# Kernel tuning notes

Hardware: AMD Instinct MI355X
Metric: run time of the kernel (lower is better)

## Reference

```python
import jax, jax.numpy as jnp
import numpy as np

N = 40000; E = 500000; IN = 128; ED = 16; HID = 64; HEADS = 4; OUT = 256; B = 128
NEG = 0.2  # GATv2 leaky_relu negative slope


def _add_self_loops(edge_index, edge_attr, n):
    # PyG add_self_loops with fill_value='mean': loop attr = mean of incoming edge attrs per node
    dst = edge_index[1]
    s = jax.ops.segment_sum(edge_attr, dst, num_segments=n)
    c = jax.ops.segment_sum(jnp.ones((edge_attr.shape[0],), edge_attr.dtype), dst, num_segments=n)
    loop_attr = s / jnp.maximum(c, 1.0)[:, None]
    loops = jnp.arange(n, dtype=edge_index.dtype)
    ei = jnp.concatenate([edge_index, jnp.stack([loops, loops])], axis=1)
    ea = jnp.concatenate([edge_attr, loop_attr], axis=0)
    return ei, ea


def _seg_softmax(logits, seg, n):
    m = jax.ops.segment_max(logits, seg, num_segments=n)
    m = jnp.where(jnp.isfinite(m), m, 0.0)  # guard empty segments
    e = jnp.exp(logits - m[seg])
    z = jax.ops.segment_sum(e, seg, num_segments=n)
    return e / (z[seg] + 1e-16)


def _gatv2(x, src, dst, ea, Wl, bl, Wr, br, We, att, bias, heads, oc, concat):
    n = x.shape[0]
    xl = (x @ Wl + bl).reshape(n, heads, oc)  # lin_l (source/message transform)
    xr = (x @ Wr + br).reshape(n, heads, oc)  # lin_r (target transform)
    ef = (ea @ We).reshape(-1, heads, oc)     # lin_edge (no bias)
    s = jax.nn.leaky_relu(xl[src] + xr[dst] + ef, NEG)  # [Etot,H,C]
    alpha = _seg_softmax(jnp.einsum('ehc,hc->eh', s, att), dst, n)  # scatter-softmax over dst
    out = jax.ops.segment_sum(xl[src] * alpha[..., None], dst, num_segments=n)  # [N,H,C]
    out = out.reshape(n, heads * oc) if concat else out.mean(axis=1)
    return out + bias


def setup_inputs():
    ks = jax.random.split(jax.random.key(0), 32)
    W = lambda i, shp: jax.random.normal(ks[i], shp, jnp.float32) * 0.05
    z = lambda d: jnp.zeros((d,), jnp.float32)
    H = HEADS * HID
    return dict(
        x=jax.random.normal(ks[0], (N, IN), jnp.float32),
        edge_index=jax.random.randint(ks[1], (2, E), 0, N),
        edge_attr=jax.random.normal(ks[2], (E, ED), jnp.float32),
        batch=jnp.sort(jax.random.randint(ks[3], (N,), 0, B)),
        batch_size=B,
        c1_Wl=W(4, (IN, H)), c1_bl=z(H), c1_Wr=W(5, (IN, H)), c1_br=z(H), c1_We=W(6, (ED, H)), c1_att=W(7, (HEADS, HID)), c1_bias=z(H),
        c2_Wl=W(8, (H, H)), c2_bl=z(H), c2_Wr=W(9, (H, H)), c2_br=z(H), c2_We=W(10, (ED, H)), c2_att=W(11, (HEADS, HID)), c2_bias=z(H),
        c3_Wl=W(12, (H, OUT)), c3_bl=z(OUT), c3_Wr=W(13, (H, OUT)), c3_br=z(OUT), c3_We=W(14, (ED, OUT)), c3_att=W(15, (1, OUT)), c3_bias=z(OUT),
        gate_W1=W(16, (OUT, 128)), gate_b1=z(128), gate_W2=W(17, (128, 1)), gate_b2=z(1),
        reg_W1=W(18, (OUT, 128)), reg_b1=z(128), reg_W2=W(19, (128, 2)), reg_b2=z(2),
    )


def reference(x, edge_index, edge_attr, batch, batch_size,
              c1_Wl, c1_bl, c1_Wr, c1_br, c1_We, c1_att, c1_bias,
              c2_Wl, c2_bl, c2_Wr, c2_br, c2_We, c2_att, c2_bias,
              c3_Wl, c3_bl, c3_Wr, c3_br, c3_We, c3_att, c3_bias,
              gate_W1, gate_b1, gate_W2, gate_b2,
              reg_W1, reg_b1, reg_W2, reg_b2):
    # task_type='homo_lumo' path; dropout disabled (inference)
    ei, ea = _add_self_loops(edge_index, edge_attr, N)
    src, dst = ei[0], ei[1]
    h = jax.nn.relu(_gatv2(x, src, dst, ea, c1_Wl, c1_bl, c1_Wr, c1_br, c1_We, c1_att, c1_bias, HEADS, HID, True))
    h = jax.nn.relu(_gatv2(h, src, dst, ea, c2_Wl, c2_bl, c2_Wr, c2_br, c2_We, c2_att, c2_bias, HEADS, HID, True))
    h = _gatv2(h, src, dst, ea, c3_Wl, c3_bl, c3_Wr, c3_br, c3_We, c3_att, c3_bias, 1, OUT, True)
    # AttentionalAggregation pooling
    gate = jax.nn.relu(h @ gate_W1 + gate_b1) @ gate_W2 + gate_b2  # [N,1]
    a = _seg_softmax(gate[:, 0], batch, batch_size)
    g = jax.ops.segment_sum(h * a[:, None], batch, num_segments=batch_size)  # [B,OUT]
    return jax.nn.relu(g @ reg_W1 + reg_b1) @ reg_W2 + reg_b2  # [B,2]
```

## Files before the change

### kernel.cpp

```cpp
#include <hip/hip_runtime.h>
#include <math.h>

constexpr int N_NODES = 40000;
constexpr int N_EDGES = 500000;
constexpr int ETOT    = N_EDGES + N_NODES;
constexpr int IN_DIM  = 128;
constexpr int ED_DIM  = 16;
constexpr int FEAT    = 256;
constexpr int BATCH   = 128;
constexpr float NEG   = 0.2f;
constexpr int NCHUNK  = (N_NODES + 255) / 256;

typedef __bf16 bf16x8 __attribute__((ext_vector_type(8)));
typedef float  f32x4  __attribute__((ext_vector_type(4)));

__global__ __launch_bounds__(256) void k_deg(const int* __restrict__ dst, int* __restrict__ deg)
{
    int e = blockIdx.x * 256 + threadIdx.x;
    if (e >= ETOT) return;
    int v = e < N_EDGES ? dst[e] : e - N_EDGES;
    atomicAdd(&deg[v], 1);
}

__global__ __launch_bounds__(256) void k_scan1(const int* __restrict__ deg, int* __restrict__ bsum)
{
    __shared__ int s[256];
    int t = threadIdx.x;
    int idx = blockIdx.x * 256 + t;
    s[t] = idx < N_NODES ? deg[idx] : 0;
    __syncthreads();
    for (int st = 128; st; st >>= 1) { if (t < st) s[t] += s[t + st]; __syncthreads(); }
    if (t == 0) bsum[blockIdx.x] = s[0];
}

__global__ __launch_bounds__(256) void k_scan2(const int* __restrict__ bsum,
    int* __restrict__ boff, int* __restrict__ rowptr)
{
    __shared__ int s[256];
    int t = threadIdx.x;
    int v = t < NCHUNK ? bsum[t] : 0;
    s[t] = v;
    __syncthreads();
    for (int off = 1; off < 256; off <<= 1) {
        int x = (t >= off) ? s[t - off] : 0;
        __syncthreads();
        s[t] += x;
        __syncthreads();
    }
    if (t < NCHUNK) boff[t] = s[t] - v;
    if (t == 0) rowptr[N_NODES] = ETOT;
}

__global__ __launch_bounds__(256) void k_scan3(const int* __restrict__ deg,
    const int* __restrict__ boff, int* __restrict__ rowptr)
{
    __shared__ int s[256];
    int t = threadIdx.x;
    int idx = blockIdx.x * 256 + t;
    int v = idx < N_NODES ? deg[idx] : 0;
    s[t] = v;
    __syncthreads();
    for (int off = 1; off < 256; off <<= 1) {
        int x = (t >= off) ? s[t - off] : 0;
        __syncthreads();
        s[t] += x;
        __syncthreads();
    }
    if (idx < N_NODES) rowptr[idx] = boff[blockIdx.x] + s[t] - v;
}

__global__ __launch_bounds__(256) void k_fill(const int* __restrict__ srcA, const int* __restrict__ dst,
    const int* __restrict__ rowptr, int* __restrict__ fill, int2* __restrict__ elist2)
{
    int e = blockIdx.x * 256 + threadIdx.x;
    if (e >= ETOT) return;
    int v = e < N_EDGES ? dst[e]  : e - N_EDGES;
    int s = e < N_EDGES ? srcA[e] : e - N_EDGES;
    int pos = rowptr[v] + atomicAdd(&fill[v], 1);
    elist2[pos] = make_int2(s, e);
}

__global__ __launch_bounds__(256) void k_loop_csr(const int2* __restrict__ elist2,
    const int* __restrict__ rowptr, const float* __restrict__ ea, float* __restrict__ loop_attr)
{
    int t = blockIdx.x * 256 + threadIdx.x;
    if (t >= N_NODES * ED_DIM) return;
    int n = t >> 4, d = t & 15;
    int p0 = rowptr[n], p1 = rowptr[n + 1];
    float s = 0.f; int c = 0;
    for (int p = p0; p < p1; ++p) {
        int e = elist2[p].y;
        if (e < N_EDGES) { s += ea[(size_t)e * ED_DIM + d]; ++c; }
    }
    loop_attr[t] = s / (float)(c > 0 ? c : 1);
}

__device__ __forceinline__ void bsplit(float x, unsigned short& h, unsigned short& l)
{
    unsigned u = __float_as_uint(x);
    unsigned r = (u + 0x7FFFu + ((u >> 16) & 1u)) >> 16;
    h = (unsigned short)r;
    float rem = x - __uint_as_float(r << 16);
    unsigned u2 = __float_as_uint(rem);
    l = (unsigned short)((u2 + 0x7FFFu + ((u2 >> 16) & 1u)) >> 16);
}

__global__ __launch_bounds__(256) void k_cvt(const float* __restrict__ X,
    unsigned short* __restrict__ Xh, unsigned short* __restrict__ Xl, int n4)
{
    int i = blockIdx.x * 256 + threadIdx.x;
    if (i >= n4) return;
    float4 v = ((const float4*)X)[i];
    ushort4 h, l;
    bsplit(v.x, h.x, l.x);
    bsplit(v.y, h.y, l.y);
    bsplit(v.z, h.z, l.z);
    bsplit(v.w, h.w, l.w);
    ((ushort4*)Xh)[i] = h;
    ((ushort4*)Xl)[i] = l;
}

__global__ __launch_bounds__(256) void k_cvtT(const float* __restrict__ W,
    unsigned short* __restrict__ WhT, unsigned short* __restrict__ WlT, int K, int N)
{
    int i = blockIdx.x * 256 + threadIdx.x;
    if (i >= K * N) return;
    int k = i / N, n = i - k * N;
    unsigned short h, l;
    bsplit(W[i], h, l);
    WhT[(size_t)n * K + k] = h;
    WlT[(size_t)n * K + k] = l;
}

__global__ __launch_bounds__(256) void k_mgemm(
    const unsigned short* __restrict__ Ah, const unsigned short* __restrict__ Al,
    const unsigned short* __restrict__ BhT, const unsigned short* __restrict__ BlT,
    const float* __restrict__ bias, float* __restrict__ C,
    int M, int N, int K, int act)
{
    int t = threadIdx.x;
    int lane = t & 63;
    int w = t >> 6;
    int mh = w >> 1, nh = w & 1;
    int bm = blockIdx.x * 128, bn = blockIdx.y * 128;
    int q = lane >> 4, lm = lane & 15;

    size_t aoff[4], boff[4];
    #pragma unroll
    for (int mt = 0; mt < 4; ++mt) {
        int r = bm + mh * 64 + mt * 16 + lm;
        r = r < M ? r : M - 1;
        aoff[mt] = (size_t)r * K + q * 8;
    }
    #pragma unroll
    for (int nt = 0; nt < 4; ++nt) {
        int c = bn + nh * 64 + nt * 16 + lm;
        boff[nt] = (size_t)c * K + q * 8;
    }

    f32x4 acc[4][4] = {};

    for (int k0 = 0; k0 < K; k0 += 32) {
        bf16x8 fah[4], fal[4], fbh[4], fbl[4];
        #pragma unroll
        for (int i = 0; i < 4; ++i) {
            fah[i] = __builtin_bit_cast(bf16x8, *(const uint4*)(Ah  + aoff[i] + k0));
            fal[i] = __builtin_bit_cast(bf16x8, *(const uint4*)(Al  + aoff[i] + k0));
            fbh[i] = __builtin_bit_cast(bf16x8, *(const uint4*)(BhT + boff[i] + k0));
            fbl[i] = __builtin_bit_cast(bf16x8, *(const uint4*)(BlT + boff[i] + k0));
        }
        #pragma unroll
        for (int mt = 0; mt < 4; ++mt)
            #pragma unroll
            for (int nt = 0; nt < 4; ++nt) {
                acc[mt][nt] = __builtin_amdgcn_mfma_f32_16x16x32_bf16(fah[mt], fbh[nt], acc[mt][nt], 0, 0, 0);
                acc[mt][nt] = __builtin_amdgcn_mfma_f32_16x16x32_bf16(fah[mt], fbl[nt], acc[mt][nt], 0, 0, 0);
                acc[mt][nt] = __builtin_amdgcn_mfma_f32_16x16x32_bf16(fal[mt], fbh[nt], acc[mt][nt], 0, 0, 0);
            }
    }

    #pragma unroll
    for (int nt = 0; nt < 4; ++nt) {
        int col = bn + nh * 64 + nt * 16 + lm;
        float bb = bias[col];
        #pragma unroll
        for (int mt = 0; mt < 4; ++mt) {
            #pragma unroll
            for (int i = 0; i < 4; ++i) {
                int row = bm + mh * 64 + mt * 16 + q * 4 + i;
                if (row < M) {
                    float o = acc[mt][nt][i] + bb;
                    if (act) o = fmaxf(o, 0.f);
                    C[(size_t)row * N + col] = o;
                }
            }
        }
    }
}

static void launch_mgemm(const unsigned short* Ah, const unsigned short* Al,
                         const unsigned short* BhT, const unsigned short* BlT,
                         const float* bias, float* C, int M, int N, int K, int act,
                         hipStream_t stream)
{
    dim3 grid((M + 127) / 128, N / 128);
    k_mgemm<<<grid, 256, 0, stream>>>(Ah, Al, BhT, BlT, bias, C, M, N, K, act);
}

#define XELOAD(s) do {                                                                \
    int src_ = __builtin_amdgcn_readfirstlane(eS[s].x);                               \
    int e_   = __builtin_amdgcn_readfirstlane(eS[s].y);                               \
    const float4* eb4_ = reinterpret_cast<const float4*>(                             \
        (e_ < N_EDGES) ? ea + (size_t)e_ * ED_DIM                                     \
                       : loop_attr + (size_t)src_ * ED_DIM);                          \
    evS[s][0] = eb4_[0]; evS[s][1] = eb4_[1];                                         \
    evS[s][2] = eb4_[2]; evS[s][3] = eb4_[3];                                         \
    xlvS[s] = *(const float4*)(xl + (size_t)src_ * FEAT + base);                      \
} while (0)

#define COMPUTE(s) do {                                                               \
    float ef0_ = 0.f, ef1_ = 0.f, ef2_ = 0.f, ef3_ = 0.f;                             \
    const float* ed_ = (const float*)evS[s];                                          \
    _Pragma("unroll")                                                                 \
    for (int d_ = 0; d_ < ED_DIM; ++d_) {                                             \
        float a_ = ed_[d_];                                                           \
        ef0_ = fmaf(a_, weR[d_].x, ef0_); ef1_ = fmaf(a_, weR[d_].y, ef1_);           \
        ef2_ = fmaf(a_, weR[d_].z, ef2_); ef3_ = fmaf(a_, weR[d_].w, ef3_);           \
    }                                                                                 \
    float s0_ = xlvS[s].x + xrv.x + ef0_;                                             \
    float s1_ = xlvS[s].y + xrv.y + ef1_;                                             \
    float s2_ = xlvS[s].z + xrv.z + ef2_;                                             \
    float s3_ = xlvS[s].w + xrv.w + ef3_;                                             \
    s0_ = fmaxf(s0_, 0.f) + NEG * fminf(s0_, 0.f);                                    \
    s1_ = fmaxf(s1_, 0.f) + NEG * fminf(s1_, 0.f);                                    \
    s2_ = fmaxf(s2_, 0.f) + NEG * fminf(s2_, 0.f);                                    \
    s3_ = fmaxf(s3_, 0.f) + NEG * fminf(s3_, 0.f);                                    \
    float l_ = fmaf(s0_, attR.x, fmaf(s1_, attR.y, fmaf(s2_, attR.z, s3_ * attR.w))); \
    l_ += __shfl_xor(l_, 1, 64);                                                      \
    l_ += __shfl_xor(l_, 2, 64);                                                      \
    l_ += __shfl_xor(l_, 4, 64);                                                      \
    l_ += __shfl_xor(l_, 8, 64);                                                      \
    if (H == 1) { l_ += __shfl_xor(l_, 16, 64); l_ += __shfl_xor(l_, 32, 64); }       \
    float nm_ = fmaxf(m, l_);                                                         \
    float sc_ = __expf(m - nm_);                                                      \
    float w_  = __expf(l_ - nm_);                                                     \
    z = fmaf(z, sc_, w_);                                                             \
    m = nm_;                                                                          \
    acc.x = fmaf(acc.x, sc_, w_ * xlvS[s].x);                                         \
    acc.y = fmaf(acc.y, sc_, w_ * xlvS[s].y);                                         \
    acc.z = fmaf(acc.z, sc_, w_ * xlvS[s].z);                                         \
    acc.w = fmaf(acc.w, sc_, w_ * xlvS[s].w);                                         \
} while (0)

template <int H, int RELU, int OUTMODE>
__global__ __launch_bounds__(256, 4) void k_gat(
    const float* __restrict__ xl, const float* __restrict__ xr,
    const float* __restrict__ ea, const float* __restrict__ loop_attr,
    const int2* __restrict__ elist2, const int* __restrict__ rowptr,
    const float* __restrict__ We, const float* __restrict__ att,
    const float* __restrict__ bias, float* __restrict__ out,
    unsigned short* __restrict__ outH, unsigned short* __restrict__ outL)
{
    int t = threadIdx.x;
    int lane = t & 63;
    int n = __builtin_amdgcn_readfirstlane(blockIdx.x * 4 + (t >> 6));
    int base = lane * 4;

    float4 weR[ED_DIM];
    #pragma unroll
    for (int d = 0; d < ED_DIM; ++d)
        weR[d] = *(const float4*)(We + d * FEAT + base);

    float4 attR = *(const float4*)(att + base);
    float4 xrv  = *(const float4*)(xr + (size_t)n * FEAT + base);

    float m = -INFINITY, z = 0.f;
    float4 acc = {0.f, 0.f, 0.f, 0.f};

    int p0 = rowptr[n], p1 = rowptr[n + 1];
    int pe = p1 - 1;

    int2   eS[2];
    float4 evS[2][4];
    float4 xlvS[2];

    eS[0] = elist2[p0];
    { int pc = p0 + 1 > pe ? pe : p0 + 1; eS[1] = elist2[pc]; }
    XELOAD(0);

    int p = p0;
    while (true) {
        XELOAD(1);
        { int pn = p + 2 > pe ? pe : p + 2; eS[0] = elist2[pn]; }
        COMPUTE(0);
        if (++p >= p1) break;
        XELOAD(0);
        { int pn = p + 2 > pe ? pe : p + 2; eS[1] = elist2[pn]; }
        COMPUTE(1);
        if (++p >= p1) break;
    }

    float inv = 1.0f / (z + 1e-16f);
    float4 bs = *(const float4*)(bias + base);
    float4 o;
    o.x = fmaf(acc.x, inv, bs.x);
    o.y = fmaf(acc.y, inv, bs.y);
    o.z = fmaf(acc.z, inv, bs.z);
    o.w = fmaf(acc.w, inv, bs.w);
    if (RELU) {
        o.x = fmaxf(o.x, 0.f); o.y = fmaxf(o.y, 0.f);
        o.z = fmaxf(o.z, 0.f); o.w = fmaxf(o.w, 0.f);
    }
    if (OUTMODE == 2)
        *(float4*)(out + (size_t)n * FEAT + base) = o;
    ushort4 oh, ol;
    bsplit(o.x, oh.x, ol.x);
    bsplit(o.y, oh.y, ol.y);
    bsplit(o.z, oh.z, ol.z);
    bsplit(o.w, oh.w, ol.w);
    *(ushort4*)(outH + (size_t)n * FEAT + base) = oh;
    *(ushort4*)(outL + (size_t)n * FEAT + base) = ol;
}

__global__ __launch_bounds__(256) void k_gate_score(const float* __restrict__ ghid,
    const float* __restrict__ W2, const float* __restrict__ b2, float* __restrict__ gate)
{
    int lane = threadIdx.x & 63;
    int n = blockIdx.x * 4 + (threadIdx.x >> 6);
    float v = ghid[(size_t)n * 128 + lane] * W2[lane] + ghid[(size_t)n * 128 + lane + 64] * W2[lane + 64];
    #pragma unroll
    for (int off = 32; off > 0; off >>= 1) v += __shfl_xor(v, off, 64);
    if (lane == 0) gate[n] = v + b2[0];
}

__device__ __forceinline__ int lbound(const int* a, int n, int v)
{
    int lo = 0, hi = n;
    while (lo < hi) { int mid = (lo + hi) >> 1; if (a[mid] < v) lo = mid + 1; else hi = mid; }
    return lo;
}

__global__ __launch_bounds__(256) void k_pool(const float* __restrict__ gate,
    const float* __restrict__ h, const int* __restrict__ batch, float* __restrict__ g)
{
    int b = blockIdx.x;
    int t = threadIdx.x;
    __shared__ float red[256];
    int start = lbound(batch, N_NODES, b);
    int end   = lbound(batch, N_NODES, b + 1);

    float mx = -INFINITY;
    for (int n = start + t; n < end; n += 256) mx = fmaxf(mx, gate[n]);
    red[t] = mx; __syncthreads();
    for (int s = 128; s; s >>= 1) { if (t < s) red[t] = fmaxf(red[t], red[t + s]); __syncthreads(); }
    float m = red[0];
    __syncthreads();

    float zs = 0.f;
    for (int n = start + t; n < end; n += 256) zs += __expf(gate[n] - m);
    red[t] = zs; __syncthreads();
    for (int s = 128; s; s >>= 1) { if (t < s) red[t] += red[t + s]; __syncthreads(); }
    float z = red[0];

    float gs = 0.f;
    for (int n = start; n < end; ++n) gs += __expf(gate[n] - m) * h[(size_t)n * FEAT + t];
    g[b * FEAT + t] = gs / (z + 1e-16f);
}

__global__ __launch_bounds__(128) void k_reg(const float* __restrict__ g,
    const float* __restrict__ W1, const float* __restrict__ b1,
    const float* __restrict__ W2, const float* __restrict__ b2, float* __restrict__ out)
{
    int b = blockIdx.x, t = threadIdx.x;
    __shared__ float sg[FEAT];
    sg[t] = g[b * FEAT + t];
    sg[t + 128] = g[b * FEAT + t + 128];
    __syncthreads();
    float hv = b1[t];
    for (int k = 0; k < FEAT; ++k) hv += sg[k] * W1[k * 128 + t];
    hv = fmaxf(hv, 0.f);
    __shared__ float p0s[128], p1s[128];
    p0s[t] = hv * W2[t * 2 + 0];
    p1s[t] = hv * W2[t * 2 + 1];
    __syncthreads();
    for (int s = 64; s; s >>= 1) {
        if (t < s) { p0s[t] += p0s[t + s]; p1s[t] += p1s[t + s]; }
        __syncthreads();
    }
    if (t == 0) { out[b * 2 + 0] = p0s[0] + b2[0]; out[b * 2 + 1] = p1s[0] + b2[1]; }
}

extern "C" void kernel_launch(void* const* d_in, const int* in_sizes, int n_in,
                              void* d_out, int out_size, void* d_ws, size_t ws_size,
                              hipStream_t stream)
{
    const float* x       = (const float*)d_in[0];
    const int*   ei      = (const int*)d_in[1];
    const float* ea      = (const float*)d_in[2];
    const int*   batch   = (const int*)d_in[3];
    const float* c1_Wl   = (const float*)d_in[5];
    const float* c1_bl   = (const float*)d_in[6];
    const float* c1_Wr   = (const float*)d_in[7];
    const float* c1_br   = (const float*)d_in[8];
    const float* c1_We   = (const float*)d_in[9];
    const float* c1_att  = (const float*)d_in[10];
    const float* c1_bias = (const float*)d_in[11];
    const float* c2_Wl   = (const float*)d_in[12];
    const float* c2_bl   = (const float*)d_in[13];
    const float* c2_Wr   = (const float*)d_in[14];
    const float* c2_br   = (const float*)d_in[15];
    const float* c2_We   = (const float*)d_in[16];
    const float* c2_att  = (const float*)d_in[17];
    const float* c2_bias = (const float*)d_in[18];
    const float* c3_Wl   = (const float*)d_in[19];
    const float* c3_bl   = (const float*)d_in[20];
    const float* c3_Wr   = (const float*)d_in[21];
    const float* c3_br   = (const float*)d_in[22];
    const float* c3_We   = (const float*)d_in[23];
    const float* c3_att  = (const float*)d_in[24];
    const float* c3_bias = (const float*)d_in[25];
    const float* gate_W1 = (const float*)d_in[26];
    const float* gate_b1 = (const float*)d_in[27];
    const float* gate_W2 = (const float*)d_in[28];
    const float* gate_b2 = (const float*)d_in[29];
    const float* reg_W1  = (const float*)d_in[30];
    const float* reg_b1  = (const float*)d_in[31];
    const float* reg_W2  = (const float*)d_in[32];
    const float* reg_b2  = (const float*)d_in[33];

    const int* srcArr = ei;
    const int* dstArr = ei + N_EDGES;

    float* ws = (float*)d_ws;
    size_t off = 0;
    auto alloc = [&](size_t nf) { float* p = ws + off; off += (nf + 63) & ~(size_t)63; return p; };
    float* xl        = alloc((size_t)N_NODES * FEAT);
    float* xr        = alloc((size_t)N_NODES * FEAT);
    float* h         = alloc((size_t)N_NODES * FEAT);
    float* loop_attr = alloc((size_t)N_NODES * ED_DIM);
    float* gpool     = alloc((size_t)BATCH * FEAT);
    unsigned short* Ah = (unsigned short*)alloc((size_t)N_NODES * FEAT / 2);
    unsigned short* Al = (unsigned short*)alloc((size_t)N_NODES * FEAT / 2);
    unsigned short* wlT_h = (unsigned short*)alloc(FEAT * FEAT / 2);
    unsigned short* wlT_l = (unsigned short*)alloc(FEAT * FEAT / 2);
    unsigned short* wrT_h = (unsigned short*)alloc(FEAT * FEAT / 2);
    unsigned short* wrT_l = (unsigned short*)alloc(FEAT * FEAT / 2);
    int* ibase  = (int*)(ws + off);
    int* deg    = ibase;
    int* fill   = ibase + N_NODES;
    int* rowptr = ibase + 2 * N_NODES;
    int* bsum   = ibase + 3 * N_NODES + 64;
    int* boff   = bsum + 256;
    int2* elist2 = (int2*)(boff + 256);

    float* ghid = xl;
    float* gate = xr;

    hipMemsetAsync(deg, 0, (size_t)2 * N_NODES * sizeof(int), stream);

    k_deg<<<(ETOT + 255) / 256, 256, 0, stream>>>(dstArr, deg);
    k_scan1<<<NCHUNK, 256, 0, stream>>>(deg, bsum);
    k_scan2<<<1, 256, 0, stream>>>(bsum, boff, rowptr);
    k_scan3<<<NCHUNK, 256, 0, stream>>>(deg, boff, rowptr);
    k_fill<<<(ETOT + 255) / 256, 256, 0, stream>>>(srcArr, dstArr, rowptr, fill, elist2);
    k_loop_csr<<<(N_NODES * ED_DIM + 255) / 256, 256, 0, stream>>>(elist2, rowptr, ea, loop_attr);

    {
        int n4 = N_NODES * IN_DIM / 4;
        k_cvt<<<(n4 + 255) / 256, 256, 0, stream>>>(x, Ah, Al, n4);
        k_cvtT<<<(IN_DIM * FEAT + 255) / 256, 256, 0, stream>>>(c1_Wl, wlT_h, wlT_l, IN_DIM, FEAT);
        k_cvtT<<<(IN_DIM * FEAT + 255) / 256, 256, 0, stream>>>(c1_Wr, wrT_h, wrT_l, IN_DIM, FEAT);
        launch_mgemm(Ah, Al, wlT_h, wlT_l, c1_bl, xl, N_NODES, FEAT, IN_DIM, 0, stream);
        launch_mgemm(Ah, Al, wrT_h, wrT_l, c1_br, xr, N_NODES, FEAT, IN_DIM, 0, stream);
    }
    k_gat<4, 1, 1><<<N_NODES / 4, 256, 0, stream>>>(xl, xr, ea, loop_attr, elist2, rowptr,
                                                    c1_We, c1_att, c1_bias, h, Ah, Al);
    {
        k_cvtT<<<(FEAT * FEAT + 255) / 256, 256, 0, stream>>>(c2_Wl, wlT_h, wlT_l, FEAT, FEAT);
        k_cvtT<<<(FEAT * FEAT + 255) / 256, 256, 0, stream>>>(c2_Wr, wrT_h, wrT_l, FEAT, FEAT);
        launch_mgemm(Ah, Al, wlT_h, wlT_l, c2_bl, xl, N_NODES, FEAT, FEAT, 0, stream);
        launch_mgemm(Ah, Al, wrT_h, wrT_l, c2_br, xr, N_NODES, FEAT, FEAT, 0, stream);
    }
    k_gat<4, 1, 1><<<N_NODES / 4, 256, 0, stream>>>(xl, xr, ea, loop_attr, elist2, rowptr,
                                                    c2_We, c2_att, c2_bias, h, Ah, Al);
    {
        k_cvtT<<<(FEAT * FEAT + 255) / 256, 256, 0, stream>>>(c3_Wl, wlT_h, wlT_l, FEAT, FEAT);
        k_cvtT<<<(FEAT * FEAT + 255) / 256, 256, 0, stream>>>(c3_Wr, wrT_h, wrT_l, FEAT, FEAT);
        launch_mgemm(Ah, Al, wlT_h, wlT_l, c3_bl, xl, N_NODES, FEAT, FEAT, 0, stream);
        launch_mgemm(Ah, Al, wrT_h, wrT_l, c3_br, xr, N_NODES, FEAT, FEAT, 0, stream);
    }
    k_gat<1, 0, 2><<<N_NODES / 4, 256, 0, stream>>>(xl, xr, ea, loop_attr, elist2, rowptr,
                                                    c3_We, c3_att, c3_bias, h, Ah, Al);

    {
        k_cvtT<<<(FEAT * 128 + 255) / 256, 256, 0, stream>>>(gate_W1, wlT_h, wlT_l, FEAT, 128);
        launch_mgemm(Ah, Al, wlT_h, wlT_l, gate_b1, ghid, N_NODES, 128, FEAT, 1, stream);
    }
    k_gate_score<<<N_NODES / 4, 256, 0, stream>>>(ghid, gate_W2, gate_b2, gate);
    k_pool<<<BATCH, 256, 0, stream>>>(gate, h, batch, gpool);
    k_reg<<<BATCH, 128, 0, stream>>>(gpool, reg_W1, reg_b1, reg_W2, reg_b2, (float*)d_out);
}
```

Before: 1.237 ms.

## Stage GEMM operand tiles through LDS with direct global-to-LDS loads

The split-bf16 MFMA GEMM previously had each wave load its A and B fragments straight from global memory, so each fragment was fetched twice, once by each of the two waves that use it. Now each wave stages a quarter of the 128x32 A and B tiles (high and low parts) into shared memory, using global_load_lds when the builtin exists. After a barrier, waves read their fragments from LDS. This halves global/L2 traffic per tile, at the cost of two barriers per k-step and no double buffering, so load latency is no longer overlapped with MFMA work.

```diff
diff --git a/kernel.cpp b/kernel.cpp
--- a/kernel.cpp
+++ b/kernel.cpp
@@ -132,12 +132,26 @@
     WlT[(size_t)n * K + k] = l;
 }
 
+
+__device__ __forceinline__ void stage16(const unsigned short* g, void* lds)
+{
+#if __has_builtin(__builtin_amdgcn_global_load_lds)
+    __builtin_amdgcn_global_load_lds(
+        (const __attribute__((address_space(1))) void*)g,
+        (__attribute__((address_space(3))) void*)lds, 16, 0, 0);
+#else
+    ((uint4*)lds)[threadIdx.x & 63] = *(const uint4*)g;
+#endif
+}
+
 __global__ __launch_bounds__(256) void k_mgemm(
     const unsigned short* __restrict__ Ah, const unsigned short* __restrict__ Al,
     const unsigned short* __restrict__ BhT, const unsigned short* __restrict__ BlT,
     const float* __restrict__ bias, float* __restrict__ C,
     int M, int N, int K, int act)
 {
+    __shared__ uint4 sAh[512], sAl[512], sBh[512], sBl[512];
+
     int t = threadIdx.x;
     int lane = t & 63;
     int w = t >> 6;
@@ -145,29 +159,41 @@
     int bm = blockIdx.x * 128, bn = blockIdx.y * 128;
     int q = lane >> 4, lm = lane & 15;
 
-    size_t aoff[4], boff[4];
-    #pragma unroll
-    for (int mt = 0; mt < 4; ++mt) {
-        int r = bm + mh * 64 + mt * 16 + lm;
-        r = r < M ? r : M - 1;
-        aoff[mt] = (size_t)r * K + q * 8;
-    }
-    #pragma unroll
-    for (int nt = 0; nt < 4; ++nt) {
-        int c = bn + nh * 64 + nt * 16 + lm;
-        boff[nt] = (size_t)c * K + q * 8;
-    }
+    int ar0 = bm + w * 16 + lm;        ar0 = ar0 < M ? ar0 : M - 1;
+    int ar1 = bm + (w + 4) * 16 + lm;  ar1 = ar1 < M ? ar1 : M - 1;
+    int bc0 = bn + w * 16 + lm;
+    int bc1 = bn + (w + 4) * 16 + lm;
+    size_t aoff0 = (size_t)ar0 * K + q * 8;
+    size_t aoff1 = (size_t)ar1 * K + q * 8;
+    size_t boff0 = (size_t)bc0 * K + q * 8;
+    size_t boff1 = (size_t)bc1 * K + q * 8;
 
     f32x4 acc[4][4] = {};
 
-    for (int k0 = 0; k0 < K; k0 += 32) {
+    int nk = K >> 5;
+    for (int ks = 0; ks < nk; ++ks) {
+        int k0 = ks << 5;
+        if (ks) __syncthreads();
+        stage16(Ah  + aoff0 + k0, &sAh[w * 64]);
+        stage16(Ah  + aoff1 + k0, &sAh[(w + 4) * 64]);
+        stage16(Al  + aoff0 + k0, &sAl[w * 64]);
+        stage16(Al  + aoff1 + k0, &sAl[(w + 4) * 64]);
+        stage16(BhT + boff0 + k0, &sBh[w * 64]);
+        stage16(BhT + boff1 + k0, &sBh[(w + 4) * 64]);
+        stage16(BlT + boff0 + k0, &sBl[w * 64]);
+        stage16(BlT + boff1 + k0, &sBl[(w + 4) * 64]);
+        __syncthreads();
+
         bf16x8 fah[4], fal[4], fbh[4], fbl[4];
         #pragma unroll
-        for (int i = 0; i < 4; ++i) {
-            fah[i] = __builtin_bit_cast(bf16x8, *(const uint4*)(Ah  + aoff[i] + k0));
-            fal[i] = __builtin_bit_cast(bf16x8, *(const uint4*)(Al  + aoff[i] + k0));
-            fbh[i] = __builtin_bit_cast(bf16x8, *(const uint4*)(BhT + boff[i] + k0));
-            fbl[i] = __builtin_bit_cast(bf16x8, *(const uint4*)(BlT + boff[i] + k0));
+        for (int mt = 0; mt < 4; ++mt) {
+            fah[mt] = __builtin_bit_cast(bf16x8, sAh[(mh * 4 + mt) * 64 + lane]);
+            fal[mt] = __builtin_bit_cast(bf16x8, sAl[(mh * 4 + mt) * 64 + lane]);
+        }
+        #pragma unroll
+        for (int nt = 0; nt < 4; ++nt) {
+            fbh[nt] = __builtin_bit_cast(bf16x8, sBh[(nh * 4 + nt) * 64 + lane]);
+            fbl[nt] = __builtin_bit_cast(bf16x8, sBl[(nh * 4 + nt) * 64 + lane]);
         }
         #pragma unroll
         for (int mt = 0; mt < 4; ++mt)
```

Result: faster. 1.037 ms (-16.1%).
